# Performance work log

Measured on AMD Instinct MI355X. Metric: run time of the kernel, lower is better.

The kernel has to match this reference:

```python
import jax, jax.numpy as jnp
import numpy as np

D_MODEL = 256; N_LEVELS = 3; N_HEADS = 8; N_POINTS = 4
BS = 4; H = 64; W = 64


def conv2d(x, w, b):
    y = jax.lax.conv_general_dilated(x, w, window_strides=(1, 1), padding='SAME',
                                     dimension_numbers=('NCHW', 'OIHW', 'NCHW'))
    return y + b[None, :, None, None]


def ms_deform_core(value, loc, attn, L, h, w):
    # value: (N, L*h*w, Hd, D); loc: (N, Lq, Hd, L, P, 2) in [0,1]; attn: (N, Lq, Hd, L, P)
    N, Len_in, Hd, D = value.shape
    v = value.reshape(N, L, h * w, Hd, D)
    # align_corners=False pixel coords, zero padding (matches MSDA CUDA kernel)
    x = loc[..., 0] * w - 0.5
    y = loc[..., 1] * h - 0.5
    x0 = jnp.floor(x); y0 = jnp.floor(y)
    lx = x - x0; ly = y - y0
    x0i = x0.astype(jnp.int32); y0i = y0.astype(jnp.int32)
    nn_ = jnp.arange(N)[:, None, None, None, None]
    hh_ = jnp.arange(Hd)[None, None, :, None, None]
    ll_ = jnp.arange(L)[None, None, None, :, None]

    def gather(xi, yi):
        valid = (xi >= 0) & (xi < w) & (yi >= 0) & (yi < h)
        pix = jnp.clip(yi, 0, h - 1) * w + jnp.clip(xi, 0, w - 1)
        g = v[nn_, ll_, pix, hh_]  # (N, Lq, Hd, L, P, D)
        return g * valid[..., None].astype(v.dtype)

    out = (gather(x0i, y0i) * ((1 - lx) * (1 - ly))[..., None]
           + gather(x0i + 1, y0i) * (lx * (1 - ly))[..., None]
           + gather(x0i, y0i + 1) * ((1 - lx) * ly)[..., None]
           + gather(x0i + 1, y0i + 1) * (lx * ly)[..., None])
    out = (out * attn[..., None]).sum(axis=(3, 4))  # (N, Lq, Hd, D)
    return out.reshape(N, -1, Hd * D)


def setup_inputs():
    key = jax.random.key(0)
    ks = jax.random.split(key, 10)
    c, L, Hd, P = D_MODEL, N_LEVELS, N_HEADS, N_POINTS
    s = 0.02
    return {
        'query': jax.random.normal(ks[0], (BS, L, c, H, W), jnp.float32),
        'reference_points': jax.random.uniform(ks[1], (BS, H * W, L, 2), jnp.float32),
        'input_flatten': jax.random.normal(ks[2], (BS, L, c, H, W), jnp.float32),
        'input_spatial_shapes': jnp.tile(jnp.array([[H, W]], jnp.int32), (L, 1)),
        'input_level_start_index': jnp.arange(L, dtype=jnp.int32) * (H * W),
        'input_padding_mask': jnp.zeros((BS, L * H * W), bool),
        'w_value': jax.random.normal(ks[3], (c, c, 3, 3), jnp.float32) * s,
        'b_value': jnp.zeros((c,), jnp.float32),
        'w_off': jax.random.normal(ks[4], (Hd * L * P * 2, L * c, 3, 3), jnp.float32) * s,
        'b_off': jax.random.normal(ks[5], (Hd * L * P * 2,), jnp.float32) * 0.1,
        'w_attn': jax.random.normal(ks[6], (Hd * L * P, L * c, 3, 3), jnp.float32) * s,
        'b_attn': jnp.zeros((Hd * L * P,), jnp.float32),
        'w_out': jax.random.normal(ks[7], (c, c, 3, 3), jnp.float32) * s,
        'b_out': jnp.zeros((c,), jnp.float32),
    }


def reference(query, reference_points, input_flatten, input_spatial_shapes,
              input_level_start_index, input_padding_mask,
              w_value, b_value, w_off, b_off, w_attn, b_attn, w_out, b_out):
    bs, t, c, h, w = query.shape
    Hd, L, P = N_HEADS, N_LEVELS, N_POINTS
    value = conv2d(input_flatten.reshape(bs * t, c, h, w), w_value, b_value)
    qmap = query.reshape(bs, t * c, h, w)
    off = conv2d(qmap, w_off, b_off)      # (bs, Hd*L*P*2, h, w)
    aw = conv2d(qmap, w_attn, b_attn)     # (bs, Hd*L*P, h, w)
    # flatten to token-major layout (matches torch flatten(3).transpose)
    value = value.reshape(bs, t, c, h * w).transpose(0, 1, 3, 2).reshape(bs, t * h * w, c)
    off = off.reshape(bs, -1, h * w).transpose(0, 2, 1)
    aw = aw.reshape(bs, -1, h * w).transpose(0, 2, 1)
    value = jnp.where(input_padding_mask[..., None], jnp.zeros((), value.dtype), value)
    value = value.reshape(bs, t * h * w, Hd, c // Hd)
    off = off.reshape(bs, h * w, Hd, L, P, 2)
    aw = jax.nn.softmax(aw.reshape(bs, h * w, Hd, L * P), axis=-1).reshape(bs, h * w, Hd, L, P)
    # normalize offsets by (W_l, H_l)
    norm = jnp.stack([input_spatial_shapes[:, 1], input_spatial_shapes[:, 0]], -1).astype(off.dtype)
    loc = reference_points[:, :, None, :, None, :] + off / norm[None, None, None, :, None, :]
    out = ms_deform_core(value, loc, aw, L, h, w)  # (bs, h*w, c)
    out = out.reshape(bs, h, w, c).transpose(0, 3, 1, 2)
    return conv2d(out, w_out, b_out)
```

## Files before the change

kernel.cpp:

```cpp
#include <hip/hip_runtime.h>

#define HW 4096
typedef __bf16 bf16_t;
typedef _Float16 f16_t;
typedef __bf16 bf16x8 __attribute__((ext_vector_type(8)));
typedef float  f32x4  __attribute__((ext_vector_type(4)));
typedef unsigned int u32;

__device__ __forceinline__ void gld_lds16(const void* g, void* l) {
    __builtin_amdgcn_global_load_lds(
        (const __attribute__((address_space(1))) u32*)g,
        (__attribute__((address_space(3))) u32*)l, 16, 0, 0);
}

__global__ void zero_border(bf16_t* __restrict__ buf, int C)
{
    const int img = blockIdx.y;
    const int c8n = C >> 3;
    int idx = blockIdx.x * 256 + threadIdx.x;
    if (idx >= 260 * c8n) return;
    int cell = idx / c8n, c8 = idx % c8n;
    int row, col;
    if (cell < 66)       { row = 0;          col = cell; }
    else if (cell < 132) { row = 65;         col = cell - 66; }
    else if (cell < 196) { row = cell - 131; col = 0; }
    else                 { row = cell - 195; col = 65; }
    *(bf16x8*)&buf[((size_t)img * 4356 + row * 66 + col) * C + c8 * 8] = (bf16x8){};
}

__global__ void prep_w(const float* __restrict__ w0, const float* __restrict__ w1,
                       bf16_t* __restrict__ out, int CIN, int CO0, int COTOT, int COPAD)
{
    int idx = blockIdx.x * 256 + threadIdx.x;
    if (idx >= COPAD * CIN) return;
    int co = idx / CIN, ci = idx % CIN;
    #pragma unroll
    for (int tap = 0; tap < 9; ++tap) {
        float v = 0.f;
        if (co < CO0)        v = w0[((size_t)co * CIN + ci) * 9 + tap];
        else if (co < COTOT) v = w1[((size_t)(co - CO0) * CIN + ci) * 9 + tap];
        out[((size_t)tap * COPAD + co) * CIN + ci] = (bf16_t)v;
    }
}

__global__ __launch_bounds__(256) void pad_nchw_to_nhwc(
    const float* __restrict__ in, bf16_t* __restrict__ out, int C)
{
    const int y = blockIdx.x, ct = blockIdx.y, img = blockIdx.z;
    const int tid = threadIdx.x;
    __shared__ float t[64][65];

    int c = tid >> 2, x0 = (tid & 3) * 16;
    const float* srcc = in + ((size_t)img * C + ct * 64 + c) * HW + y * 64 + x0;
    #pragma unroll
    for (int j = 0; j < 4; ++j) {
        float4 v = *(const float4*)&srcc[j * 4];
        t[c][x0 + j * 4 + 0] = v.x; t[c][x0 + j * 4 + 1] = v.y;
        t[c][x0 + j * 4 + 2] = v.z; t[c][x0 + j * 4 + 3] = v.w;
    }
    __syncthreads();
    int x = tid >> 2, cg = (tid & 3) * 16;
    bf16_t tmp[16];
    #pragma unroll
    for (int j = 0; j < 16; ++j) tmp[j] = (bf16_t)t[cg + j][x];
    bf16_t* dst = &out[((size_t)img * 4356 + (size_t)((y + 1) * 66 + (x + 1))) * C + ct * 64 + cg];
    *(bf16x8*)dst       = *(bf16x8*)&tmp[0];
    *((bf16x8*)dst + 1) = *(bf16x8*)&tmp[8];
}

template<int CIN, int MODE>
__global__ __launch_bounds__(256) void mfma_conv(
    const bf16_t* __restrict__ Apad,
    const bf16_t* __restrict__ Wprep,
    const float* __restrict__ bias0,
    const float* __restrict__ bias1,
    const unsigned char* __restrict__ mask,
    void* __restrict__ outp)
{
    constexpr int NCHUNK = CIN / 64;
    constexpr int COPAD = (MODE == 1) ? 320 : 256;

    const int gy = gridDim.y;
    const int nwg = 32 * gy * gridDim.z;
    const int pb = blockIdx.x + 32 * (blockIdx.y + gy * blockIdx.z);
    const int lb = (pb & 7) * (nwg >> 3) + (pb >> 3);
    const int bx  = lb & 31;
    const int by  = (lb >> 5) % gy;
    const int img = lb / (32 * gy);

    const int tid = threadIdx.x;
    const int l = tid & 63;
    const int w = tid >> 6;
    const int wm = w >> 1, wn = w & 1;
    const int y0 = bx * 2;
    const int cobase = by * 64;

    __shared__ bf16_t ldsA[4 * 66 * 64];
    __shared__ bf16_t ldsB[2][64 * 64];

    const bf16_t* Aimg = Apad + (size_t)img * (66 * 66) * CIN;

    f32x4 acc[4][2];
    #pragma unroll
    for (int m = 0; m < 4; ++m)
        #pragma unroll
        for (int n = 0; n < 2; ++n) acc[m][n] = (f32x4){0.f, 0.f, 0.f, 0.f};

    auto stageA = [&](int ci0) {
        for (int i = w; i < 33; i += 4) {
            int s = i * 64 + l;
            int row = s / 528;
            int rem = s - row * 528;
            int col = rem >> 3, qs = rem & 7;
            int qsrc = qs ^ (col & 7);
            const bf16_t* src = Aimg + ((size_t)((y0 + row) * 66 + col)) * CIN + ci0 + qsrc * 8;
            gld_lds16(src, &ldsA[i * 512]);
        }
    };
    auto stageB = [&](int tap, int ci0, int bufsel) {
        #pragma unroll
        for (int i = 0; i < 2; ++i) {
            int s = (w * 2 + i) * 64 + l;
            int r = s >> 3, qs = s & 7;
            int qsrc = qs ^ (r & 7);
            const bf16_t* src = Wprep + ((size_t)tap * COPAD + cobase + r) * CIN + ci0 + qsrc * 8;
            gld_lds16(src, &ldsB[bufsel][(w * 2 + i) * 512]);
        }
    };

    auto rdA = [&](int dy, int dx, int m, int kk) -> bf16x8 {
        int col = m * 16 + (l & 15) + dx;
        int kq = kk * 4 + (l >> 4);
        float4 v = *(const float4*)&ldsA[((wm + dy) * 66 + col) * 64 + ((kq ^ (col & 7)) * 8)];
        return __builtin_bit_cast(bf16x8, v);
    };
    auto rdB = [&](int bufsel, int n, int kk) -> bf16x8 {
        int r = wn * 32 + n * 16 + (l & 15);
        int kq = kk * 4 + (l >> 4);
        float4 v = *(const float4*)&ldsB[bufsel][r * 64 + ((kq ^ (r & 7)) * 8)];
        return __builtin_bit_cast(bf16x8, v);
    };

    for (int chunk = 0; chunk < NCHUNK; ++chunk) {
        const int ci0 = chunk * 64;
        stageA(ci0);
        stageB(0, ci0, 0);
        __syncthreads();

        int buf = 0;
        for (int tap = 0; tap < 9; ++tap) {
            const int dy = tap / 3, dx = tap % 3;
            if (tap < 8) stageB(tap + 1, ci0, buf ^ 1);
            #pragma unroll
            for (int kk = 0; kk < 2; ++kk) {
                bf16x8 a0 = rdA(dy, dx, 0, kk), a1 = rdA(dy, dx, 1, kk);
                bf16x8 a2 = rdA(dy, dx, 2, kk), a3 = rdA(dy, dx, 3, kk);
                bf16x8 b0 = rdB(buf, 0, kk), b1 = rdB(buf, 1, kk);
                #pragma unroll
                for (int m = 0; m < 4; ++m) {
                    bf16x8 am = (m == 0) ? a0 : (m == 1) ? a1 : (m == 2) ? a2 : a3;
                    if constexpr (MODE == 2) {
                        acc[m][0] = __builtin_amdgcn_mfma_f32_16x16x32_bf16(b0, am, acc[m][0], 0, 0, 0);
                        acc[m][1] = __builtin_amdgcn_mfma_f32_16x16x32_bf16(b1, am, acc[m][1], 0, 0, 0);
                    } else {
                        acc[m][0] = __builtin_amdgcn_mfma_f32_16x16x32_bf16(am, b0, acc[m][0], 0, 0, 0);
                        acc[m][1] = __builtin_amdgcn_mfma_f32_16x16x32_bf16(am, b1, acc[m][1], 0, 0, 0);
                    }
                }
            }
            __syncthreads();
            buf ^= 1;
        }
    }

    #pragma unroll
    for (int m = 0; m < 4; ++m)
        #pragma unroll
        for (int n = 0; n < 2; ++n) {
            f32x4 fr = acc[m][n];
            if constexpr (MODE == 2) {
                int co  = cobase + wn * 32 + n * 16 + (l >> 4) * 4;
                int pix = bx * 128 + wm * 64 + m * 16 + (l & 15);
                float* op = (float*)outp;
                #pragma unroll
                for (int r = 0; r < 4; ++r)
                    op[((size_t)img * 256 + co + r) * HW + pix] = fr[r] + bias0[co + r];
            } else {
                int pix = bx * 128 + wm * 64 + m * 16 + (l >> 4) * 4;
                int co  = cobase + wn * 32 + n * 16 + (l & 15);
                if constexpr (MODE == 0) {
                    bf16_t* op = (bf16_t*)outp;
                    float bv = bias0[co];
                    #pragma unroll
                    for (int r = 0; r < 4; ++r) {
                        int p = pix + r;
                        float vv = fr[r] + bv;
                        if (mask[(size_t)img * HW + p]) vv = 0.f;
                        op[((size_t)img * HW + p) * 256 + co] = (bf16_t)vv;
                    }
                } else {
                    if (co < 288) {
                        f16_t* op = (f16_t*)outp;
                        float bv = (co < 192) ? bias0[co] : bias1[co - 192];
                        #pragma unroll
                        for (int r = 0; r < 4; ++r)
                            op[((size_t)img * HW + pix + r) * 288 + co] = (f16_t)(fr[r] + bv);
                    }
                }
            }
        }
}

__global__ __launch_bounds__(256) void msda_core_kernel(
    const bf16_t* __restrict__ value,
    const f16_t* __restrict__ offattn,
    const float* __restrict__ refp,
    bf16_t* __restrict__ outpad)
{
    constexpr int QB = 16;
    const int n    = blockIdx.y;
    const int q0   = blockIdx.x * QB;
    const int tid  = threadIdx.x;
    const int oct  = tid & 31;
    const int qsub = tid >> 5;
    const int hd   = oct >> 2;

    __shared__ float s_oa[QB][288];
    __shared__ float s_ref[QB][6];
    __shared__ float s_aw[QB][96];

    for (int e = tid; e < QB * 288; e += 256) {
        int q = e / 288, c = e % 288;
        s_oa[q][c] = (float)offattn[((size_t)n * HW + q0 + q) * 288 + c];
    }
    if (tid < QB * 6) {
        int q = tid / 6, r = tid % 6;
        s_ref[q][r] = refp[((size_t)n * HW + q0 + q) * 6 + r];
    }
    __syncthreads();

    if (tid < QB * 8) {
        int q = tid >> 3, h = tid & 7;
        const float* a = &s_oa[q][192 + h * 12];
        float mx = a[0];
        #pragma unroll
        for (int k = 1; k < 12; ++k) mx = fmaxf(mx, a[k]);
        float e[12]; float sum = 0.f;
        #pragma unroll
        for (int k = 0; k < 12; ++k) { e[k] = __expf(a[k] - mx); sum += e[k]; }
        float inv = 1.f / sum;
        #pragma unroll
        for (int k = 0; k < 12; ++k) s_aw[q][h * 12 + k] = e[k] * inv;
    }
    __syncthreads();

    float acc[2][8];
    #pragma unroll
    for (int qi = 0; qi < 2; ++qi)
        #pragma unroll
        for (int j = 0; j < 8; ++j) acc[qi][j] = 0.f;

    const bf16x8 zero8 = {};
    const size_t vstride = (size_t)HW * 256;
    const bf16_t* vimg = value + (size_t)(n * 3) * vstride + oct * 8;

    auto issue = [&](int pt, bf16x8 (&g)[2][4], float (&wt)[2][4]) {
        const int ll = pt >> 2, p = pt & 3;
        const bf16_t* vbase = vimg + (size_t)ll * vstride;
        #pragma unroll
        for (int qi = 0; qi < 2; ++qi) {
            const int qq = qsub * 2 + qi;
            const int idx = hd * 12 + ll * 4 + p;
            float x = s_ref[qq][ll * 2 + 0] * 64.f - 0.5f + s_oa[qq][idx * 2 + 0];
            float y = s_ref[qq][ll * 2 + 1] * 64.f - 0.5f + s_oa[qq][idx * 2 + 1];
            float aw = s_aw[qq][idx];
            float xf = floorf(x), yf = floorf(y);
            float lx = x - xf, ly = y - yf;
            int xi = (int)xf, yi = (int)yf;
            wt[qi][0] = (1.f - lx) * (1.f - ly) * aw;
            wt[qi][1] = lx * (1.f - ly) * aw;
            wt[qi][2] = (1.f - lx) * ly * aw;
            wt[qi][3] = lx * ly * aw;
            bool vx0 = (xi >= 0) && (xi < 64);
            bool vx1 = (xi + 1 >= 0) && (xi + 1 < 64);
            bool vy0 = (yi >= 0) && (yi < 64);
            bool vy1 = (yi + 1 >= 0) && (yi + 1 < 64);
            g[qi][0] = (vy0 && vx0) ? *(const bf16x8*)(vbase + (size_t)(yi * 64 + xi) * 256)           : zero8;
            g[qi][1] = (vy0 && vx1) ? *(const bf16x8*)(vbase + (size_t)(yi * 64 + xi + 1) * 256)       : zero8;
            g[qi][2] = (vy1 && vx0) ? *(const bf16x8*)(vbase + (size_t)((yi + 1) * 64 + xi) * 256)     : zero8;
            g[qi][3] = (vy1 && vx1) ? *(const bf16x8*)(vbase + (size_t)((yi + 1) * 64 + xi + 1) * 256) : zero8;
        }
    };
    auto consume = [&](bf16x8 (&g)[2][4], float (&wt)[2][4]) {
        #pragma unroll
        for (int qi = 0; qi < 2; ++qi)
            #pragma unroll
            for (int j = 0; j < 8; ++j)
                acc[qi][j] += wt[qi][0] * (float)g[qi][0][j] + wt[qi][1] * (float)g[qi][1][j]
                            + wt[qi][2] * (float)g[qi][2][j] + wt[qi][3] * (float)g[qi][3][j];
    };

    bf16x8 gA[2][4], gB[2][4];
    float  wA[2][4], wB[2][4];
    issue(0, gA, wA);
    #pragma unroll 1
    for (int pt = 0; pt < 12; pt += 2) {
        if (pt + 1 < 12) issue(pt + 1, gB, wB);
        consume(gA, wA);
        if (pt + 2 < 12) issue(pt + 2, gA, wA);
        consume(gB, wB);
    }

    #pragma unroll
    for (int qi = 0; qi < 2; ++qi) {
        const int qq = qsub * 2 + qi;
        int pix = q0 + qq;
        int pp = ((pix >> 6) + 1) * 66 + (pix & 63) + 1;
        bf16_t tmp[8];
        #pragma unroll
        for (int j = 0; j < 8; ++j) tmp[j] = (bf16_t)acc[qi][j];
        *(bf16x8*)&outpad[((size_t)n * 4356 + pp) * 256 + oct * 8] = *(bf16x8*)tmp;
    }
}

extern "C" void kernel_launch(void* const* d_in, const int* in_sizes, int n_in,
                              void* d_out, int out_size, void* d_ws, size_t ws_size,
                              hipStream_t stream) {
    const float* query   = (const float*)d_in[0];
    const float* refp    = (const float*)d_in[1];
    const float* inflat  = (const float*)d_in[2];
    const unsigned char* mask = (const unsigned char*)d_in[5];
    const float* w_value = (const float*)d_in[6];
    const float* b_value = (const float*)d_in[7];
    const float* w_off   = (const float*)d_in[8];
    const float* b_off   = (const float*)d_in[9];
    const float* w_attn  = (const float*)d_in[10];
    const float* b_attn  = (const float*)d_in[11];
    const float* w_out   = (const float*)d_in[12];
    const float* b_out   = (const float*)d_in[13];

    char* ws = (char*)d_ws;
    bf16_t* A_val  = (bf16_t*)ws;  ws += (size_t)12 * 4356 * 256 * 2;
    bf16_t* A_qry  = (bf16_t*)ws;  ws += (size_t)4 * 4356 * 768 * 2;
    bf16_t* A_core = (bf16_t*)ws;  ws += (size_t)4 * 4356 * 256 * 2;
    bf16_t* W_val  = (bf16_t*)ws;  ws += (size_t)9 * 256 * 256 * 2;
    bf16_t* W_off  = (bf16_t*)ws;  ws += (size_t)9 * 320 * 768 * 2;
    bf16_t* W_out  = (bf16_t*)ws;  ws += (size_t)9 * 256 * 256 * 2;
    f16_t*  offattn = (f16_t*)ws;  ws += (size_t)4 * 4096 * 288 * 2;
    bf16_t* value  = A_qry;

    zero_border<<<dim3(33, 12), 256, 0, stream>>>(A_val, 256);
    zero_border<<<dim3(98, 4),  256, 0, stream>>>(A_qry, 768);
    zero_border<<<dim3(33, 4),  256, 0, stream>>>(A_core, 256);

    prep_w<<<(256 * 256 + 255) / 256, 256, 0, stream>>>(w_value, nullptr, W_val, 256, 256, 256, 256);
    prep_w<<<(320 * 768 + 255) / 256, 256, 0, stream>>>(w_off, w_attn, W_off, 768, 192, 288, 320);
    prep_w<<<(256 * 256 + 255) / 256, 256, 0, stream>>>(w_out, nullptr, W_out, 256, 256, 256, 256);

    pad_nchw_to_nhwc<<<dim3(64, 4, 12), 256, 0, stream>>>(inflat, A_val, 256);
    pad_nchw_to_nhwc<<<dim3(64, 12, 4), 256, 0, stream>>>(query,  A_qry, 768);

    mfma_conv<768, 1><<<dim3(32, 5, 4),  256, 0, stream>>>(A_qry, W_off, b_off, b_attn, nullptr, offattn);
    mfma_conv<256, 0><<<dim3(32, 4, 12), 256, 0, stream>>>(A_val, W_val, b_value, nullptr, mask, value);

    msda_core_kernel<<<dim3(HW / 16, 4), 256, 0, stream>>>(value, offattn, refp, A_core);

    mfma_conv<256, 2><<<dim3(32, 4, 4),  256, 0, stream>>>(A_core, W_out, b_out, nullptr, nullptr, d_out);
}
```

Before: 263.1 us.

## Triple-buffer conv weight taps with explicit waitcnt and MFMA priority scheduling

Expands the weight LDS buffer from two to three slots so that each tap prefetches the weight tile two taps ahead instead of one. The single __syncthreads is replaced with explicit vmcnt/lgkmcnt waits, raw s_barriers and a sched_barrier. All LDS fragment reads are hoisted ahead of the MFMA block, which runs at raised wave priority. The aim is to hide global-to-LDS latency and keep the matrix units busy, at the cost of more LDS per block (which may reduce occupancy) and fragile hand-written wait counts.

```diff
diff --git a/kernel.cpp b/kernel.cpp
--- a/kernel.cpp
+++ b/kernel.cpp
@@ -96,7 +96,7 @@
     const int cobase = by * 64;
 
     __shared__ bf16_t ldsA[4 * 66 * 64];
-    __shared__ bf16_t ldsB[2][64 * 64];
+    __shared__ bf16_t ldsB[3][64 * 64];
 
     const bf16_t* Aimg = Apad + (size_t)img * (66 * 66) * CIN;
 
@@ -145,31 +145,65 @@
         const int ci0 = chunk * 64;
         stageA(ci0);
         stageB(0, ci0, 0);
+        stageB(1, ci0, 1);
         __syncthreads();
 
-        int buf = 0;
         for (int tap = 0; tap < 9; ++tap) {
             const int dy = tap / 3, dx = tap % 3;
-            if (tap < 8) stageB(tap + 1, ci0, buf ^ 1);
-            #pragma unroll
-            for (int kk = 0; kk < 2; ++kk) {
-                bf16x8 a0 = rdA(dy, dx, 0, kk), a1 = rdA(dy, dx, 1, kk);
-                bf16x8 a2 = rdA(dy, dx, 2, kk), a3 = rdA(dy, dx, 3, kk);
-                bf16x8 b0 = rdB(buf, 0, kk), b1 = rdB(buf, 1, kk);
-                #pragma unroll
-                for (int m = 0; m < 4; ++m) {
-                    bf16x8 am = (m == 0) ? a0 : (m == 1) ? a1 : (m == 2) ? a2 : a3;
-                    if constexpr (MODE == 2) {
-                        acc[m][0] = __builtin_amdgcn_mfma_f32_16x16x32_bf16(b0, am, acc[m][0], 0, 0, 0);
-                        acc[m][1] = __builtin_amdgcn_mfma_f32_16x16x32_bf16(b1, am, acc[m][1], 0, 0, 0);
-                    } else {
-                        acc[m][0] = __builtin_amdgcn_mfma_f32_16x16x32_bf16(am, b0, acc[m][0], 0, 0, 0);
-                        acc[m][1] = __builtin_amdgcn_mfma_f32_16x16x32_bf16(am, b1, acc[m][1], 0, 0, 0);
-                    }
-                }
+            const int rb = tap % 3;
+            bf16x8 a00 = rdA(dy, dx, 0, 0), a10 = rdA(dy, dx, 1, 0);
+            bf16x8 a20 = rdA(dy, dx, 2, 0), a30 = rdA(dy, dx, 3, 0);
+            bf16x8 a01 = rdA(dy, dx, 0, 1), a11 = rdA(dy, dx, 1, 1);
+            bf16x8 a21 = rdA(dy, dx, 2, 1), a31 = rdA(dy, dx, 3, 1);
+            bf16x8 b00 = rdB(rb, 0, 0), b10 = rdB(rb, 1, 0);
+            bf16x8 b01 = rdB(rb, 0, 1), b11 = rdB(rb, 1, 1);
+            if (tap < 7) {
+                stageB(tap + 2, ci0, (tap + 2) % 3);
+                asm volatile("s_waitcnt vmcnt(2)" ::: "memory");
+            } else {
+                asm volatile("s_waitcnt vmcnt(0)" ::: "memory");
             }
-            __syncthreads();
-            buf ^= 1;
+            __builtin_amdgcn_s_barrier();
+            asm volatile("s_waitcnt lgkmcnt(0)" ::: "memory");
+            __builtin_amdgcn_sched_barrier(0);
+            __builtin_amdgcn_s_setprio(1);
+            if constexpr (MODE == 2) {
+                acc[0][0] = __builtin_amdgcn_mfma_f32_16x16x32_bf16(b00, a00, acc[0][0], 0, 0, 0);
+                acc[0][1] = __builtin_amdgcn_mfma_f32_16x16x32_bf16(b10, a00, acc[0][1], 0, 0, 0);
+                acc[1][0] = __builtin_amdgcn_mfma_f32_16x16x32_bf16(b00, a10, acc[1][0], 0, 0, 0);
+                acc[1][1] = __builtin_amdgcn_mfma_f32_16x16x32_bf16(b10, a10, acc[1][1], 0, 0, 0);
+                acc[2][0] = __builtin_amdgcn_mfma_f32_16x16x32_bf16(b00, a20, acc[2][0], 0, 0, 0);
+                acc[2][1] = __builtin_amdgcn_mfma_f32_16x16x32_bf16(b10, a20, acc[2][1], 0, 0, 0);
+                acc[3][0] = __builtin_amdgcn_mfma_f32_16x16x32_bf16(b00, a30, acc[3][0], 0, 0, 0);
+                acc[3][1] = __builtin_amdgcn_mfma_f32_16x16x32_bf16(b10, a30, acc[3][1], 0, 0, 0);
+                acc[0][0] = __builtin_amdgcn_mfma_f32_16x16x32_bf16(b01, a01, acc[0][0], 0, 0, 0);
+                acc[0][1] = __builtin_amdgcn_mfma_f32_16x16x32_bf16(b11, a01, acc[0][1], 0, 0, 0);
+                acc[1][0] = __builtin_amdgcn_mfma_f32_16x16x32_bf16(b01, a11, acc[1][0], 0, 0, 0);
+                acc[1][1] = __builtin_amdgcn_mfma_f32_16x16x32_bf16(b11, a11, acc[1][1], 0, 0, 0);
+                acc[2][0] = __builtin_amdgcn_mfma_f32_16x16x32_bf16(b01, a21, acc[2][0], 0, 0, 0);
+                acc[2][1] = __builtin_amdgcn_mfma_f32_16x16x32_bf16(b11, a21, acc[2][1], 0, 0, 0);
+                acc[3][0] = __builtin_amdgcn_mfma_f32_16x16x32_bf16(b01, a31, acc[3][0], 0, 0, 0);
+                acc[3][1] = __builtin_amdgcn_mfma_f32_16x16x32_bf16(b11, a31, acc[3][1], 0, 0, 0);
+            } else {
+                acc[0][0] = __builtin_amdgcn_mfma_f32_16x16x32_bf16(a00, b00, acc[0][0], 0, 0, 0);
+                acc[0][1] = __builtin_amdgcn_mfma_f32_16x16x32_bf16(a00, b10, acc[0][1], 0, 0, 0);
+                acc[1][0] = __builtin_amdgcn_mfma_f32_16x16x32_bf16(a10, b00, acc[1][0], 0, 0, 0);
+                acc[1][1] = __builtin_amdgcn_mfma_f32_16x16x32_bf16(a10, b10, acc[1][1], 0, 0, 0);
+                acc[2][0] = __builtin_amdgcn_mfma_f32_16x16x32_bf16(a20, b00, acc[2][0], 0, 0, 0);
+                acc[2][1] = __builtin_amdgcn_mfma_f32_16x16x32_bf16(a20, b10, acc[2][1], 0, 0, 0);
+                acc[3][0] = __builtin_amdgcn_mfma_f32_16x16x32_bf16(a30, b00, acc[3][0], 0, 0, 0);
+                acc[3][1] = __builtin_amdgcn_mfma_f32_16x16x32_bf16(a30, b10, acc[3][1], 0, 0, 0);
+                acc[0][0] = __builtin_amdgcn_mfma_f32_16x16x32_bf16(a01, b01, acc[0][0], 0, 0, 0);
+                acc[0][1] = __builtin_amdgcn_mfma_f32_16x16x32_bf16(a01, b11, acc[0][1], 0, 0, 0);
+                acc[1][0] = __builtin_amdgcn_mfma_f32_16x16x32_bf16(a11, b01, acc[1][0], 0, 0, 0);
+                acc[1][1] = __builtin_amdgcn_mfma_f32_16x16x32_bf16(a11, b11, acc[1][1], 0, 0, 0);
+                acc[2][0] = __builtin_amdgcn_mfma_f32_16x16x32_bf16(a21, b01, acc[2][0], 0, 0, 0);
+                acc[2][1] = __builtin_amdgcn_mfma_f32_16x16x32_bf16(a21, b11, acc[2][1], 0, 0, 0);
+                acc[3][0] = __builtin_amdgcn_mfma_f32_16x16x32_bf16(a31, b01, acc[3][0], 0, 0, 0);
+                acc[3][1] = __builtin_amdgcn_mfma_f32_16x16x32_bf16(a31, b11, acc[3][1], 0, 0, 0);
+            }
+            __builtin_amdgcn_s_setprio(0);
+            __builtin_amdgcn_s_barrier();
         }
     }
 
```

Measured after the change: 292.9 us. +11.3%, slower.
